# Performance work log

Hardware: AMD Instinct MI355X
Metric: run time of the kernel (lower is better)

## Reference

```python
import jax, jax.numpy as jnp
import numpy as np

N_BINS = 32
R = 1.2
BOUND = 50.0
_m = N_BINS // 2
_x1L = BOUND * (R - 1.0) / (R ** _m - 1.0)
X1L = _x1L / (2.0 * BOUND)  # x1L rescaled to the [0,1] domain
_idx = np.arange(N_BINS + 1, dtype=np.float64) - _m
_xr = np.where(_idx >= 0, (1.0 - R ** _idx) / (1.0 - R), (1.0 - R ** np.abs(_idx)) / (1.0 - R))
_xr = np.where(_idx >= 0, _x1L * _xr, -_x1L * _xr)
_xr = (_xr + BOUND) / (2.0 * BOUND)
MESH = np.concatenate([[0.0], _xr[1:-1], [1.0]]).astype(np.float32)   # (n_bins+1,)
ESIZE = (MESH[1:] - MESH[:-1]).astype(np.float32)                     # (n_bins,)

N, D = 524288, 64

def setup_inputs() -> dict:
    key = jax.random.key(0)
    k1, k2, k3, k4 = jax.random.split(key, 4)
    return {
        "x": jax.random.normal(k1, (N, D), jnp.float32) * 5.0,
        "logdet": jnp.zeros((N, 1), jnp.float32),
        "p": jax.random.normal(k2, (N_BINS - 1, D), jnp.float32) * 0.1,
        "b": jax.random.normal(k3, (1, D), jnp.float32) * 0.1,
        "logs": jax.random.normal(k4, (1, D), jnp.float32) * 0.1,
    }

def reference(x, logdet, p, b, logs):
    mesh = jnp.asarray(MESH)              # (n_bins+1,)
    es = jnp.asarray(ESIZE)               # (n_bins,)
    # ---- actnorm (data_init already done; b_init = logs_init = 0) ----
    ls = jnp.clip(logs, -5.0, 5.0)
    z = (x + b) * jnp.exp(ls)             # (N, D)
    logdet = logdet + jnp.sum(ls)
    # ---- pdf normalization ----
    ep = jnp.exp(p)                                         # (n_bins-1, D)
    w = ((es[:-1] + es[1:]) / 2.0)[:, None]                 # trapezoid weights
    px = ep * ((1.0 - es[0]) / jnp.sum(ep * w, 0, keepdims=True))
    ones = jnp.ones((1, p.shape[1]), p.dtype)
    pdf = jnp.concatenate([ones, px, ones], 0)              # (n_bins+1, D)
    cell = (pdf[:-1] + pdf[1:]) / 2.0 * es[:, None]         # (n_bins, D)
    F_ref = jnp.concatenate([jnp.zeros_like(ones), jnp.cumsum(cell, 0)[:-1]], 0)  # (n_bins, D)
    # ---- forward CDF: analytic bin index + batched gather + quadratic interp ----
    xs = (z + BOUND) / (2.0 * BOUND)                        # map to [0,1]
    sgn = jnp.sign(xs - 0.5)
    mfl = jnp.floor(jnp.log(jnp.abs(xs - 0.5) * (R - 1.0) / X1L + 1.0) / np.log(R))
    k = jnp.where(sgn >= 0, N_BINS // 2 + mfl, N_BINS // 2 - mfl - 1).astype(jnp.int32)
    cover = (k * (k - (N_BINS - 1))) <= 0                   # inside the mesh?
    k = jnp.clip(k, 0, N_BINS - 1)
    v1 = jnp.take_along_axis(pdf, k, 0)                     # pdf at left node
    v2 = jnp.take_along_axis(pdf, k + 1, 0)                 # pdf at right node
    xmodi = xs - mesh[k]
    h = es[k]
    F_pre = jnp.take_along_axis(F_ref, k, 0)
    y = jnp.where(cover, F_pre + xmodi * xmodi * 0.5 * (v2 - v1) / h + xmodi * v1, xs)
    dlog = jnp.where(cover, xmodi * (v2 - v1) / h + v1, 1.0)
    logdet = logdet + jnp.sum(jnp.log(dlog), axis=1, keepdims=True)
    out = y * 2.0 * BOUND - BOUND
    return out, logdet
```

## Files before the change

### kernel.cpp

```cpp
#include <hip/hip_runtime.h>
#include <math.h>

#define NBINS 32
#define DCOLS 64

#define WS_A     0
#define WS_B     2048
#define WS_C     4096
#define WS_S     6144
#define WS_T     6208
#define WS_SUMLS 6272

__global__ __launch_bounds__(64) void precompute_kernel(
    const float* __restrict__ p, const float* __restrict__ b,
    const float* __restrict__ logs, float* __restrict__ ws)
{
  const int d = threadIdx.x;

  double powr[17];
  {
    double rp = 1.0;
    for (int i = 0; i <= 16; i++) { powr[i] = rp; rp *= 1.2; }
  }
  const double x1L = 50.0 * 0.2 / (powr[16] - 1.0);
  float meshf[NBINS + 1];
  for (int i = 0; i <= NBINS; i++) {
    int idx = i - 16;
    int a = idx >= 0 ? idx : -idx;
    double xr = (1.0 - powr[a]) / (1.0 - 1.2);
    xr = (idx >= 0) ? x1L * xr : -x1L * xr;
    meshf[i] = (float)((xr + 50.0) / 100.0);
  }
  meshf[0] = 0.0f;
  meshf[NBINS] = 1.0f;
  float esf[NBINS];
  for (int i = 0; i < NBINS; i++) esf[i] = meshf[i + 1] - meshf[i];

  float ls = logs[d];
  ls = fminf(fmaxf(ls, -5.0f), 5.0f);
  const float s = expf(ls);
  const float bd = b[d];

  float ep[NBINS - 1];
  float denom = 0.0f;
  for (int j = 0; j < NBINS - 1; j++) {
    ep[j] = expf(p[j * DCOLS + d]);
    denom += ep[j] * ((esf[j] + esf[j + 1]) * 0.5f);
  }
  const float fnorm = (1.0f - esf[0]) / denom;
  float pdf[NBINS + 1];
  pdf[0] = 1.0f;
  pdf[NBINS] = 1.0f;
  for (int j = 0; j < NBINS - 1; j++) pdf[j + 1] = ep[j] * fnorm;

  float F = 0.0f;
  for (int k = 0; k < NBINS; k++) {
    const double v1 = (double)pdf[k];
    const double v2 = (double)pdf[k + 1];
    const double h  = (double)esf[k];
    const double m  = (double)meshf[k];
    const double c2 = 0.5 * (v2 - v1) / h;
    const double c1 = v1;
    const double A  = (double)F - c1 * m + c2 * m * m;
    const double B  = c1 - 2.0 * c2 * m;
    ws[WS_A + k * DCOLS + d] = (float)A;
    ws[WS_B + k * DCOLS + d] = (float)B;
    ws[WS_C + k * DCOLS + d] = (float)c2;
    const float cell = 0.5f * (pdf[k] + pdf[k + 1]) * esf[k];
    F += cell;
  }

  ws[WS_S + d] = (float)((double)s * 0.01);
  ws[WS_T + d] = (float)((double)bd * (double)s * 0.01 + 0.5);

  float sum = ls;
  for (int m = 1; m < 64; m <<= 1) sum += __shfl_xor(sum, m, 64);
  if (d == 0) ws[WS_SUMLS] = sum;
}

__global__ __launch_bounds__(256) void fwd_kernel(
    const float* __restrict__ x, const float* __restrict__ logdet_in,
    const float* __restrict__ ws, float* __restrict__ out,
    float* __restrict__ logdet_out, int nrows, float C1, float INVLNR)
{
  __shared__ float sA[NBINS * DCOLS];
  __shared__ float sB[NBINS * DCOLS];
  __shared__ float sC[NBINS * DCOLS];
  for (int i = threadIdx.x; i < NBINS * DCOLS; i += 256) {
    sA[i] = ws[WS_A + i];
    sB[i] = ws[WS_B + i];
    sC[i] = ws[WS_C + i];
  }
  const int lane = threadIdx.x & 63;
  const int wid  = threadIdx.x >> 6;
  const float S     = ws[WS_S + lane];
  const float T     = ws[WS_T + lane];
  const float sumls = ws[WS_SUMLS];
  __syncthreads();

  const int gw = blockIdx.x * 4 + wid;
  const int nw = gridDim.x * 4;

  for (int r0 = gw * 4; r0 < nrows; r0 += nw * 4) {
    float res[4], prod[4];
#pragma unroll
    for (int j = 0; j < 4; j++) {
      const int r = r0 + j;
      const float xv = x[(size_t)r * DCOLS + lane];
      const float xs = fmaf(xv, S, T);
      const float a  = fabsf(xs - 0.5f);
      const float u  = logf(fmaf(a, C1, 1.0f)) * INVLNR;
      const float mfl = floorf(u);
      const float kf  = (xs >= 0.5f) ? (16.0f + mfl) : (15.0f - mfl);
      const int k = (int)kf;
      const bool cover = (k >= 0) && (k <= NBINS - 1);
      int kc = k < 0 ? 0 : (k > NBINS - 1 ? NBINS - 1 : k);
      const int idx = kc * DCOLS + lane;
      const float Av = sA[idx];
      const float Bv = sB[idx];
      const float Cv = sC[idx];
      const float y  = cover ? fmaf(xs, fmaf(xs, Cv, Bv), Av) : xs;
      const float dl = cover ? fmaf(xs, 2.0f * Cv, Bv) : 1.0f;
      res[j]  = fmaf(y, 100.0f, -50.0f);
      prod[j] = dl;
    }
#pragma unroll
    for (int j = 0; j < 4; j++)
      out[(size_t)(r0 + j) * DCOLS + lane] = res[j];

#pragma unroll
    for (int j = 0; j < 4; j++) {
      float pr = prod[j];
      for (int m = 1; m < 64; m <<= 1) pr *= __shfl_xor(pr, m, 64);
      prod[j] = pr;
    }
    float pr = prod[0];
    pr = (lane == 1) ? prod[1] : pr;
    pr = (lane == 2) ? prod[2] : pr;
    pr = (lane == 3) ? prod[3] : pr;
    if (lane < 4) {
      const int r = r0 + lane;
      logdet_out[r] = logdet_in[r] + sumls + logf(pr);
    }
  }
}

extern "C" void kernel_launch(void* const* d_in, const int* in_sizes, int n_in,
                              void* d_out, int out_size, void* d_ws, size_t ws_size,
                              hipStream_t stream) {
  const float* x      = (const float*)d_in[0];
  const float* logdet = (const float*)d_in[1];
  const float* p      = (const float*)d_in[2];
  const float* b      = (const float*)d_in[3];
  const float* logs   = (const float*)d_in[4];
  float* out = (float*)d_out;
  float* ws  = (float*)d_ws;

  const int N = in_sizes[0] / DCOLS;
  float* logdet_out = out + (size_t)N * DCOLS;

  precompute_kernel<<<1, 64, 0, stream>>>(p, b, logs, ws);

  double Rm = 1.0;
  for (int i = 0; i < 16; i++) Rm *= 1.2;
  const double x1L = 50.0 * (1.2 - 1.0) / (Rm - 1.0);
  const double X1L = x1L / 100.0;
  const float C1     = (float)((1.2 - 1.0) / X1L);
  const float INVLNR = (float)(1.0 / log(1.2));

  const int grid = 2048;
  fwd_kernel<<<grid, 256, 0, stream>>>(x, logdet, ws, out, logdet_out, N,
                                       C1, INVLNR);
}
```

Measured before the change: 311.0 us.

## Vectorize forward kernel with float4 row loads and shorter product reductions

Each lane now handles four adjacent columns through float4 loads and stores, and each wave covers eight rows per iteration instead of four. This cuts the number of memory instructions and shortens the cross-lane product reduction from six shuffle steps to four. The natural log is replaced with the fast hardware __log2f scaled by 1/log2(R). The risk is a slightly different bin index at bin boundaries from the lower-precision log, and four-way LDS bank conflicts on the per-lane table gathers.

```diff
diff --git a/kernel.cpp b/kernel.cpp
--- a/kernel.cpp
+++ b/kernel.cpp
@@ -78,69 +78,93 @@
   if (d == 0) ws[WS_SUMLS] = sum;
 }
 
+__device__ __forceinline__ void proc4(
+    const float4 xv, const float4 S4, const float4 T4,
+    const float* __restrict__ sA, const float* __restrict__ sB,
+    const float* __restrict__ sC, int c0, float C1, float INVL2R,
+    float4& res, float& prod)
+{
+  float xs_[4] = { fmaf(xv.x, S4.x, T4.x), fmaf(xv.y, S4.y, T4.y),
+                   fmaf(xv.z, S4.z, T4.z), fmaf(xv.w, S4.w, T4.w) };
+  float r_[4];
+  float pr = 1.0f;
+#pragma unroll
+  for (int i = 0; i < 4; i++) {
+    const float xs = xs_[i];
+    const float a  = fabsf(xs - 0.5f);
+    const float u  = __log2f(fmaf(a, C1, 1.0f)) * INVL2R;
+    const float mfl = floorf(u);
+    const float kf  = (xs >= 0.5f) ? (16.0f + mfl) : (15.0f - mfl);
+    const int k = (int)kf;
+    const bool cover = (k >= 0) && (k <= NBINS - 1);
+    const int kc = k < 0 ? 0 : (k > NBINS - 1 ? NBINS - 1 : k);
+    const int idx = kc * DCOLS + c0 + i;
+    const float Av = sA[idx];
+    const float Bv = sB[idx];
+    const float Cv = sC[idx];
+    const float y  = cover ? fmaf(xs, fmaf(xs, Cv, Bv), Av) : xs;
+    const float dl = cover ? fmaf(xs, 2.0f * Cv, Bv) : 1.0f;
+    r_[i] = fmaf(y, 100.0f, -50.0f);
+    pr *= dl;
+  }
+  res = make_float4(r_[0], r_[1], r_[2], r_[3]);
+  prod = pr;
+}
+
 __global__ __launch_bounds__(256) void fwd_kernel(
     const float* __restrict__ x, const float* __restrict__ logdet_in,
     const float* __restrict__ ws, float* __restrict__ out,
-    float* __restrict__ logdet_out, int nrows, float C1, float INVLNR)
+    float* __restrict__ logdet_out, int nrows, float C1, float INVL2R)
 {
   __shared__ float sA[NBINS * DCOLS];
   __shared__ float sB[NBINS * DCOLS];
   __shared__ float sC[NBINS * DCOLS];
-  for (int i = threadIdx.x; i < NBINS * DCOLS; i += 256) {
-    sA[i] = ws[WS_A + i];
-    sB[i] = ws[WS_B + i];
-    sC[i] = ws[WS_C + i];
+  {
+    const float4* wsv = (const float4*)(ws);
+    float4* sAv = (float4*)sA;
+    float4* sBv = (float4*)sB;
+    float4* sCv = (float4*)sC;
+    for (int i = threadIdx.x; i < (NBINS * DCOLS) / 4; i += 256) {
+      sAv[i] = wsv[(WS_A / 4) + i];
+      sBv[i] = wsv[(WS_B / 4) + i];
+      sCv[i] = wsv[(WS_C / 4) + i];
+    }
   }
   const int lane = threadIdx.x & 63;
   const int wid  = threadIdx.x >> 6;
-  const float S     = ws[WS_S + lane];
-  const float T     = ws[WS_T + lane];
+  const int cg   = lane & 15;
+  const int rs   = lane >> 4;
+  const int c0   = cg * 4;
+  const float4 S4 = *(const float4*)(ws + WS_S + c0);
+  const float4 T4 = *(const float4*)(ws + WS_T + c0);
   const float sumls = ws[WS_SUMLS];
   __syncthreads();
 
   const int gw = blockIdx.x * 4 + wid;
   const int nw = gridDim.x * 4;
 
-  for (int r0 = gw * 4; r0 < nrows; r0 += nw * 4) {
-    float res[4], prod[4];
-#pragma unroll
-    for (int j = 0; j < 4; j++) {
-      const int r = r0 + j;
-      const float xv = x[(size_t)r * DCOLS + lane];
-      const float xs = fmaf(xv, S, T);
-      const float a  = fabsf(xs - 0.5f);
-      const float u  = logf(fmaf(a, C1, 1.0f)) * INVLNR;
-      const float mfl = floorf(u);
-      const float kf  = (xs >= 0.5f) ? (16.0f + mfl) : (15.0f - mfl);
-      const int k = (int)kf;
-      const bool cover = (k >= 0) && (k <= NBINS - 1);
-      int kc = k < 0 ? 0 : (k > NBINS - 1 ? NBINS - 1 : k);
-      const int idx = kc * DCOLS + lane;
-      const float Av = sA[idx];
-      const float Bv = sB[idx];
-      const float Cv = sC[idx];
-      const float y  = cover ? fmaf(xs, fmaf(xs, Cv, Bv), Av) : xs;
-      const float dl = cover ? fmaf(xs, 2.0f * Cv, Bv) : 1.0f;
-      res[j]  = fmaf(y, 100.0f, -50.0f);
-      prod[j] = dl;
-    }
-#pragma unroll
-    for (int j = 0; j < 4; j++)
-      out[(size_t)(r0 + j) * DCOLS + lane] = res[j];
+  for (int r0 = gw * 8; r0 < nrows; r0 += nw * 8) {
+    const int rA = r0 + rs;
+    const int rB = r0 + 4 + rs;
+    const float4 xA = *(const float4*)(x + (size_t)rA * DCOLS + c0);
+    const float4 xB = *(const float4*)(x + (size_t)rB * DCOLS + c0);
+
+    float4 resA, resB;
+    float pA, pB;
+    proc4(xA, S4, T4, sA, sB, sC, c0, C1, INVL2R, resA, pA);
+    proc4(xB, S4, T4, sA, sB, sC, c0, C1, INVL2R, resB, pB);
+
+    *(float4*)(out + (size_t)rA * DCOLS + c0) = resA;
+    *(float4*)(out + (size_t)rB * DCOLS + c0) = resB;
 
 #pragma unroll
-    for (int j = 0; j < 4; j++) {
-      float pr = prod[j];
-      for (int m = 1; m < 64; m <<= 1) pr *= __shfl_xor(pr, m, 64);
-      prod[j] = pr;
+    for (int m = 1; m < 16; m <<= 1) {
+      pA *= __shfl_xor(pA, m, 64);
+      pB *= __shfl_xor(pB, m, 64);
     }
-    float pr = prod[0];
-    pr = (lane == 1) ? prod[1] : pr;
-    pr = (lane == 2) ? prod[2] : pr;
-    pr = (lane == 3) ? prod[3] : pr;
-    if (lane < 4) {
-      const int r = r0 + lane;
-      logdet_out[r] = logdet_in[r] + sumls + logf(pr);
+    if (cg == 0) {
+      logdet_out[rA] = logdet_in[rA] + sumls + logf(pA);
+      logdet_out[rB] = logdet_in[rB] + sumls + logf(pB);
     }
   }
 }
@@ -165,10 +189,10 @@
   for (int i = 0; i < 16; i++) Rm *= 1.2;
   const double x1L = 50.0 * (1.2 - 1.0) / (Rm - 1.0);
   const double X1L = x1L / 100.0;
-  const float C1     = (float)((1.2 - 1.0) / X1L);
-  const float INVLNR = (float)(1.0 / log(1.2));
+  const float C1      = (float)((1.2 - 1.0) / X1L);
+  const float INVL2R  = (float)(1.0 / log2(1.2));
 
   const int grid = 2048;
   fwd_kernel<<<grid, 256, 0, stream>>>(x, logdet, ws, out, logdet_out, N,
-                                       C1, INVLNR);
+                                       C1, INVL2R);
 }
```

Result: faster. 250.9 us (-19.3%).
